# Kernel optimization log

Hardware: AMD Instinct MI355X
Metric: run time of the kernel (lower is better)

The kernel has to match this reference:

```python
import jax, jax.numpy as jnp
import numpy as np
from jax import lax

# Poincare ball, curvature c = 1.0 (geoopt default for CustomPoincare)
SQRT_C = 1.0
BALL_EPS = 1e-3   # projx margin (geoopt-style)
MIN_NORM = 1e-7
BN_EPS = 1e-5


def _norm(x):
    # norm over channel (last) dim, clamped away from 0
    return jnp.maximum(jnp.linalg.norm(x, axis=-1, keepdims=True), MIN_NORM)


def projx(x):
    # clip points back inside the ball of radius (1-eps)/sqrt(c)
    maxnorm = (1.0 - BALL_EPS) / SQRT_C
    n = _norm(x)
    return x * jnp.minimum(1.0, maxnorm / n)


def expmap0(v):
    # exp map at the origin: tanh(sqrt(c)||v||) * v / (sqrt(c)||v||)
    n = _norm(v)
    return projx(jnp.tanh(SQRT_C * n) * v / (SQRT_C * n))


def logmap0(x):
    # log map at the origin: artanh(sqrt(c)||x||) * x / (sqrt(c)||x||)
    n = _norm(x)
    t = jnp.minimum(SQRT_C * n, 1.0 - 1e-5)
    return jnp.arctanh(t) * x / (SQRT_C * n)


def setup_inputs() -> dict:
    key = jax.random.key(0)
    k0, k1 = jax.random.split(key)
    B, C_in, H, W, C_out = 16, 3, 224, 224, 64
    x = jax.random.normal(k0, (B, C_in, H, W), dtype=jnp.float32)
    # Kaiming-ish init for the 3x3 stem conv, HWIO layout
    fan_in = 3 * 3 * C_in
    conv_w = jax.random.normal(k1, (3, 3, C_in, C_out), dtype=jnp.float32) * np.float32(np.sqrt(2.0 / fan_in))
    conv_b = jnp.zeros((C_out,), dtype=jnp.float32)
    bn_gamma = jnp.ones((C_out,), dtype=jnp.float32)
    bn_beta = jnp.zeros((C_out,), dtype=jnp.float32)
    return {"x": x, "conv_w": conv_w, "conv_b": conv_b,
            "bn_gamma": bn_gamma, "bn_beta": bn_beta}


def reference(x, conv_w, conv_b, bn_gamma, bn_beta):
    # x: [B, C, H, W] -> NHWC (channel-last points on the Poincare ball)
    h = jnp.transpose(x, (0, 2, 3, 1))
    h = projx(h)

    # --- PoincareConv2d: tangent-space 3x3 conv (log0 -> conv+bias -> exp0) ---
    u = logmap0(h)
    u = lax.conv_general_dilated(
        u, conv_w, window_strides=(1, 1), padding="SAME",
        dimension_numbers=("NHWC", "HWIO", "NHWC"))
    u = u + conv_b
    h = expmap0(u)

    # --- PoincareBatchNorm2d: tangent-space BN over (B,H,W) per channel ---
    u = logmap0(h)
    mean = jnp.mean(u, axis=(0, 1, 2), keepdims=True)
    var = jnp.var(u, axis=(0, 1, 2), keepdims=True)
    u = (u - mean) * lax.rsqrt(var + BN_EPS) * bn_gamma + bn_beta
    h = expmap0(u)

    # --- PoincareTangentReLU ---
    h = expmap0(jax.nn.relu(logmap0(h)))
    return h  # [B, H, W, C_out]
```

## Files before the change

### kernel.cpp

```cpp
#include <hip/hip_runtime.h>
#include <math.h>

#define B_ 16
#define H_ 224
#define W_ 224
#define HP_ 226
#define WP_ 226
#define CIN_ 3
#define COUT_ 64
#define NPIX_ (B_ * H_ * W_)
#define NPAD_ (B_ * HP_ * WP_)
#define NBLK_ (NPIX_ / 256)
#define MAXNORM_ 0.999f
#define MINN_ 1e-7f
#define TCL_ (1.0f - 1e-5f)
#define LCLAMP_ 3.8002012f
#define BN_EPS_ 1e-5f
#define NF_ ((float)NPIX_)
#define PADW2_ 36

typedef float v4f __attribute__((ext_vector_type(4)));

struct Acc {
  v4f v0, v1, v2, v3, v4, v5, v6, v7, v8, v9, v10, v11, v12, v13, v14, v15;
};

#define EACH16(X) X(0) X(1) X(2) X(3) X(4) X(5) X(6) X(7) \
                  X(8) X(9) X(10) X(11) X(12) X(13) X(14) X(15)
#define EACH8LO(X) X(0) X(1) X(2) X(3) X(4) X(5) X(6) X(7)
#define EACH8HI(X) X(8) X(9) X(10) X(11) X(12) X(13) X(14) X(15)

__global__ void k0_transform(const float* __restrict__ x, float4* __restrict__ u0p) {
  int idx = blockIdx.x * 256 + threadIdx.x;
  if (idx >= NPAD_) return;
  int b = idx / (HP_ * WP_);
  int r = idx % (HP_ * WP_);
  int yp = r / WP_, xp = r % WP_;
  float4 o = make_float4(0.f, 0.f, 0.f, 0.f);
  if (yp >= 1 && yp <= H_ && xp >= 1 && xp <= W_) {
    const float* xb = x + (size_t)b * (CIN_ * H_ * W_) + (size_t)(yp - 1) * W_ + (xp - 1);
    float v0 = xb[0];
    float v1 = xb[H_ * W_];
    float v2 = xb[2 * H_ * W_];
    float n = sqrtf(fmaf(v0, v0, fmaf(v1, v1, v2 * v2)));
    float ncl = fmaxf(n, MINN_);
    float s = fminf(1.0f, MAXNORM_ / ncl);
    float p0 = v0 * s, p1 = v1 * s, p2 = v2 * s;
    float np_ = fmaxf(sqrtf(fmaf(p0, p0, fmaf(p1, p1, p2 * p2))), MINN_);
    float t = fminf(np_, TCL_);
    float ath = 0.5f * __logf(__fdividef(1.0f + t, 1.0f - t));
    float f = __fdividef(ath, np_);
    o.x = p0 * f; o.y = p1 * f; o.z = p2 * f;
  }
  u0p[idx] = o;
}

__device__ __forceinline__ void conv_clamp(const float4* __restrict__ u0p,
                                           const float* __restrict__ wgt,
                                           const float* __restrict__ bias,
                                           int pix, Acc& a) {
  int b = pix / (H_ * W_);
  int r = pix % (H_ * W_);
  int y = r / W_, x = r % W_;
  const float4* base = u0p + ((size_t)b * HP_ + y) * WP_ + x;
  const v4f* b4 = (const v4f*)bias;
#define INIT(i) a.v##i = b4[i];
  EACH16(INIT)
#undef INIT
#define FMA_X(i) a.v##i += in.x * wp[i];
#define FMA_Y(i) a.v##i += in.y * wp[16 + i];
#define FMA_Z(i) a.v##i += in.z * wp[32 + i];
#define TAP(t) { float4 in = base[((t) / 3) * WP_ + ((t) % 3)];              \
                 const v4f* wp = (const v4f*)(wgt + (t) * 3 * COUT_);        \
                 EACH16(FMA_X) EACH16(FMA_Y) EACH16(FMA_Z) }
  TAP(0) TAP(1) TAP(2) TAP(3) TAP(4) TAP(5) TAP(6) TAP(7) TAP(8)
#undef TAP
#undef FMA_X
#undef FMA_Y
#undef FMA_Z
  v4f s2 = (v4f)0.0f;
#define SQ(i) s2 += a.v##i * a.v##i;
  EACH16(SQ)
#undef SQ
  float n2 = s2.x + s2.y + s2.z + s2.w;
  float n = sqrtf(n2);
  float sc = (n > LCLAMP_) ? (LCLAMP_ / n) : 1.0f;
#define SCL(i) a.v##i *= sc;
  EACH16(SCL)
}

__global__ void __launch_bounds__(256, 4)
k1_stats(const float4* __restrict__ u0p, const float* __restrict__ wgt,
         const float* __restrict__ bias, float* __restrict__ partials) {
  int pix = blockIdx.x * 256 + threadIdx.x;
  Acc a;
  conv_clamp(u0p, wgt, bias, pix, a);

  __shared__ __align__(16) float stg[4 * 64 * PADW2_];
  __shared__ float red[512];
  int lane = threadIdx.x & 63, wid = threadIdx.x >> 6;
  float* row = stg + (size_t)(wid * 64 + lane) * PADW2_;
  int c = lane & 31, half = lane >> 5;
  const float* col = stg + ((size_t)wid * 64 + half * 32) * PADW2_ + c;

#define STGA(i) *(v4f*)(row + 4 * (i)) = a.v##i;
  EACH8LO(STGA)
#undef STGA
  __builtin_amdgcn_wave_barrier();
  float sA0 = 0.f, sA1 = 0.f, qA0 = 0.f, qA1 = 0.f;
#pragma unroll
  for (int p = 0; p < 32; p += 2) {
    float a0 = col[(p + 0) * PADW2_];
    float a1 = col[(p + 1) * PADW2_];
    sA0 += a0; qA0 = fmaf(a0, a0, qA0);
    sA1 += a1; qA1 = fmaf(a1, a1, qA1);
  }
  float sA = sA0 + sA1, qA = qA0 + qA1;
  __builtin_amdgcn_wave_barrier();

#define STGB(i) *(v4f*)(row + 4 * ((i) - 8)) = a.v##i;
  EACH8HI(STGB)
#undef STGB
  __builtin_amdgcn_wave_barrier();
  float sB0 = 0.f, sB1 = 0.f, qB0 = 0.f, qB1 = 0.f;
#pragma unroll
  for (int p = 0; p < 32; p += 2) {
    float a0 = col[(p + 0) * PADW2_];
    float a1 = col[(p + 1) * PADW2_];
    sB0 += a0; qB0 = fmaf(a0, a0, qB0);
    sB1 += a1; qB1 = fmaf(a1, a1, qB1);
  }
  float sB = sB0 + sB1, qB = qB0 + qB1;

  sA += __shfl_xor(sA, 32, 64);  qA += __shfl_xor(qA, 32, 64);
  sB += __shfl_xor(sB, 32, 64);  qB += __shfl_xor(qB, 32, 64);

  if (lane < 32) {
    red[0 * 128 + wid * 32 + c] = sA;
    red[1 * 128 + wid * 32 + c] = sB;
    red[2 * 128 + wid * 32 + c] = qA;
    red[3 * 128 + wid * 32 + c] = qB;
  }
  __syncthreads();
  int tid = threadIdx.x;
  if (tid < 128) {
    int base = (tid >> 5) * 128 + (tid & 31);
    float tot = red[base] + red[base + 32] + red[base + 64] + red[base + 96];
    partials[(size_t)blockIdx.x * 128 + tid] = tot;
  }
}

__global__ void k2_finalize(const float* __restrict__ partials, const float* __restrict__ gamma,
                            float* __restrict__ stats) {
  int c = blockIdx.x;
  int t = threadIdx.x;
  float s = 0.f, q = 0.f;
  for (int i = t; i < NBLK_; i += 256) {
    s += partials[(size_t)i * 128 + c];
    q += partials[(size_t)i * 128 + 64 + c];
  }
  __shared__ float ls[256], lq[256];
  ls[t] = s; lq[t] = q;
  __syncthreads();
#pragma unroll
  for (int off = 128; off > 0; off >>= 1) {
    if (t < off) { ls[t] += ls[t + off]; lq[t] += lq[t + off]; }
    __syncthreads();
  }
  if (t == 0) {
    float mean = ls[0] / NF_;
    float msq  = lq[0] / NF_;
    float var = msq - mean * mean;
    stats[c] = mean;
    stats[64 + c] = gamma[c] / sqrtf(var + BN_EPS_);
  }
}

__global__ void __launch_bounds__(256, 4)
k3_final(const float4* __restrict__ u0p, const float* __restrict__ wgt,
         const float* __restrict__ bias, const float* __restrict__ stats,
         const float* __restrict__ beta, float* __restrict__ out) {
  int pix = blockIdx.x * 256 + threadIdx.x;
  Acc a;
  conv_clamp(u0p, wgt, bias, pix, a);
  const v4f* mean4 = (const v4f*)stats;
  const v4f* rg4   = (const v4f*)(stats + 64);
  const v4f* beta4 = (const v4f*)beta;
  v4f s2 = (v4f)0.0f;
#define BN(i) { a.v##i = (a.v##i - mean4[i]) * rg4[i] + beta4[i]; s2 += a.v##i * a.v##i; }
  EACH16(BN)
#undef BN
  float nv2 = s2.x + s2.y + s2.z + s2.w;
  float nv = sqrtf(nv2);
  float sv = (nv > LCLAMP_) ? (LCLAMP_ / nv) : 1.0f;
  v4f z2 = (v4f)0.0f;
#define RELU(i) { v4f r = a.v##i * sv;                                      \
                  r.x = fmaxf(r.x, 0.f); r.y = fmaxf(r.y, 0.f);             \
                  r.z = fmaxf(r.z, 0.f); r.w = fmaxf(r.w, 0.f);             \
                  a.v##i = r; z2 += r * r; }
  EACH16(RELU)
#undef RELU
  float nw2 = z2.x + z2.y + z2.z + z2.w;
  float nw = fmaxf(sqrtf(nw2), MINN_);
  float e2 = __expf(2.0f * nw);
  float th = 1.0f - __fdividef(2.0f, e2 + 1.0f);
  float se = __fdividef(th, nw);
  float clip = fminf(1.0f, MAXNORM_ / fmaxf(th, MINN_));
  float fs = se * clip;

  __shared__ __align__(16) float stg[4 * 64 * PADW2_];
  int lane = threadIdx.x & 63, wid = threadIdx.x >> 6;
  float* row = stg + (size_t)(wid * 64 + lane) * PADW2_;
  int pr8 = lane >> 3, qi = lane & 7;
  const float* rb = stg + (size_t)wid * 64 * PADW2_ + pr8 * PADW2_ + qi * 4;
  v4f* outw = (v4f*)out + ((size_t)blockIdx.x * 256 + wid * 64) * 16;

#define STGA(i) *(v4f*)(row + 4 * (i)) = a.v##i * fs;
  EACH8LO(STGA)
#undef STGA
  __builtin_amdgcn_wave_barrier();
#pragma unroll
  for (int j = 0; j < 8; j++) {
    v4f v = *(const v4f*)(rb + j * 8 * PADW2_);
    __builtin_nontemporal_store(v, outw + (j * 8 + pr8) * 16 + qi);
  }
  __builtin_amdgcn_wave_barrier();

#define STGB(i) *(v4f*)(row + 4 * ((i) - 8)) = a.v##i * fs;
  EACH8HI(STGB)
#undef STGB
  __builtin_amdgcn_wave_barrier();
#pragma unroll
  for (int j = 0; j < 8; j++) {
    v4f v = *(const v4f*)(rb + j * 8 * PADW2_);
    __builtin_nontemporal_store(v, outw + (j * 8 + pr8) * 16 + 8 + qi);
  }
}

extern "C" void kernel_launch(void* const* d_in, const int* in_sizes, int n_in,
                              void* d_out, int out_size, void* d_ws, size_t ws_size,
                              hipStream_t stream) {
  const float* x     = (const float*)d_in[0];
  const float* wgt   = (const float*)d_in[1];
  const float* bias  = (const float*)d_in[2];
  const float* gamma = (const float*)d_in[3];
  const float* beta  = (const float*)d_in[4];
  float* out = (float*)d_out;

  char* ws = (char*)d_ws;
  float4* u0p      = (float4*)ws;
  float*  partials = (float*)(ws + (size_t)NPAD_ * 16);
  float*  stats    = (float*)(ws + (size_t)NPAD_ * 16 + (size_t)NBLK_ * 128 * 4);

  hipLaunchKernelGGL(k0_transform, dim3((NPAD_ + 255) / 256), dim3(256), 0, stream, x, u0p);
  hipLaunchKernelGGL(k1_stats,     dim3(NBLK_),               dim3(256), 0, stream, u0p, wgt, bias, partials);
  hipLaunchKernelGGL(k2_finalize,  dim3(64),                  dim3(256), 0, stream, partials, gamma, stats);
  hipLaunchKernelGGL(k3_final,     dim3(NBLK_),               dim3(256), 0, stream, u0p, wgt, bias, stats, beta, out);
}
```

Measured before the change: 307.9 us.

## Materialize clamped conv output in workspace instead of recomputing conv in final pass

The stats kernel now writes the clamped tangent-space conv result to a workspace buffer, and a new final kernel reads that buffer rather than re-running the 3x3 conv. The stats reduction is also reworked to read from the transposed staging layout with vector shuffles. This swaps repeated conv compute for an extra 205MB write plus read of global memory. A fallback keeps the recompute path when the workspace is too small.

```diff
diff --git a/kernel.cpp b/kernel.cpp
--- a/kernel.cpp
+++ b/kernel.cpp
@@ -89,63 +89,77 @@
   EACH16(SCL)
 }
 
+__device__ __forceinline__ v4f vshfl_xor(v4f v, int m) {
+  v4f r;
+  r.x = __shfl_xor(v.x, m, 64);
+  r.y = __shfl_xor(v.y, m, 64);
+  r.z = __shfl_xor(v.z, m, 64);
+  r.w = __shfl_xor(v.w, m, 64);
+  return r;
+}
+
+template <bool STORE_T>
 __global__ void __launch_bounds__(256, 4)
 k1_stats(const float4* __restrict__ u0p, const float* __restrict__ wgt,
-         const float* __restrict__ bias, float* __restrict__ partials) {
+         const float* __restrict__ bias, float* __restrict__ tbuf,
+         float* __restrict__ partials) {
   int pix = blockIdx.x * 256 + threadIdx.x;
   Acc a;
   conv_clamp(u0p, wgt, bias, pix, a);
 
   __shared__ __align__(16) float stg[4 * 64 * PADW2_];
-  __shared__ float red[512];
+  __shared__ float red_s[256], red_q[256];
   int lane = threadIdx.x & 63, wid = threadIdx.x >> 6;
   float* row = stg + (size_t)(wid * 64 + lane) * PADW2_;
-  int c = lane & 31, half = lane >> 5;
-  const float* col = stg + ((size_t)wid * 64 + half * 32) * PADW2_ + c;
+  int pr8 = lane >> 3, qi = lane & 7;
+  const float* rb = stg + (size_t)wid * 64 * PADW2_ + pr8 * PADW2_ + qi * 4;
+  v4f* outw = (v4f*)tbuf + ((size_t)blockIdx.x * 256 + wid * 64) * 16;
 
 #define STGA(i) *(v4f*)(row + 4 * (i)) = a.v##i;
   EACH8LO(STGA)
 #undef STGA
   __builtin_amdgcn_wave_barrier();
-  float sA0 = 0.f, sA1 = 0.f, qA0 = 0.f, qA1 = 0.f;
-#pragma unroll
-  for (int p = 0; p < 32; p += 2) {
-    float a0 = col[(p + 0) * PADW2_];
-    float a1 = col[(p + 1) * PADW2_];
-    sA0 += a0; qA0 = fmaf(a0, a0, qA0);
-    sA1 += a1; qA1 = fmaf(a1, a1, qA1);
-  }
-  float sA = sA0 + sA1, qA = qA0 + qA1;
+  v4f sA = (v4f)0.0f, qA = (v4f)0.0f;
+#pragma unroll
+  for (int j = 0; j < 8; j++) {
+    v4f v = *(const v4f*)(rb + j * 8 * PADW2_);
+    if (STORE_T) __builtin_nontemporal_store(v, outw + (j * 8 + pr8) * 16 + qi);
+    sA += v; qA += v * v;
+  }
+  sA += vshfl_xor(sA, 8);  qA += vshfl_xor(qA, 8);
+  sA += vshfl_xor(sA, 16); qA += vshfl_xor(qA, 16);
+  sA += vshfl_xor(sA, 32); qA += vshfl_xor(qA, 32);
+  if (lane < 8) {
+    *(v4f*)&red_s[wid * 32 + qi * 4] = sA;
+    *(v4f*)&red_q[wid * 32 + qi * 4] = qA;
+  }
   __builtin_amdgcn_wave_barrier();
 
 #define STGB(i) *(v4f*)(row + 4 * ((i) - 8)) = a.v##i;
   EACH8HI(STGB)
 #undef STGB
   __builtin_amdgcn_wave_barrier();
-  float sB0 = 0.f, sB1 = 0.f, qB0 = 0.f, qB1 = 0.f;
-#pragma unroll
-  for (int p = 0; p < 32; p += 2) {
-    float a0 = col[(p + 0) * PADW2_];
-    float a1 = col[(p + 1) * PADW2_];
-    sB0 += a0; qB0 = fmaf(a0, a0, qB0);
-    sB1 += a1; qB1 = fmaf(a1, a1, qB1);
-  }
-  float sB = sB0 + sB1, qB = qB0 + qB1;
-
-  sA += __shfl_xor(sA, 32, 64);  qA += __shfl_xor(qA, 32, 64);
-  sB += __shfl_xor(sB, 32, 64);  qB += __shfl_xor(qB, 32, 64);
-
-  if (lane < 32) {
-    red[0 * 128 + wid * 32 + c] = sA;
-    red[1 * 128 + wid * 32 + c] = sB;
-    red[2 * 128 + wid * 32 + c] = qA;
-    red[3 * 128 + wid * 32 + c] = qB;
+  v4f sB = (v4f)0.0f, qB = (v4f)0.0f;
+#pragma unroll
+  for (int j = 0; j < 8; j++) {
+    v4f v = *(const v4f*)(rb + j * 8 * PADW2_);
+    if (STORE_T) __builtin_nontemporal_store(v, outw + (j * 8 + pr8) * 16 + 8 + qi);
+    sB += v; qB += v * v;
+  }
+  sB += vshfl_xor(sB, 8);  qB += vshfl_xor(qB, 8);
+  sB += vshfl_xor(sB, 16); qB += vshfl_xor(qB, 16);
+  sB += vshfl_xor(sB, 32); qB += vshfl_xor(qB, 32);
+  if (lane < 8) {
+    *(v4f*)&red_s[128 + wid * 32 + qi * 4] = sB;
+    *(v4f*)&red_q[128 + wid * 32 + qi * 4] = qB;
   }
   __syncthreads();
   int tid = threadIdx.x;
   if (tid < 128) {
-    int base = (tid >> 5) * 128 + (tid & 31);
-    float tot = red[base] + red[base + 32] + red[base + 64] + red[base + 96];
+    int c = tid & 63;
+    int base = (c >> 5) * 128 + (c & 31);
+    const float* rr = (tid < 64) ? red_s : red_q;
+    float tot = rr[base] + rr[base + 32] + rr[base + 64] + rr[base + 96];
     partials[(size_t)blockIdx.x * 128 + tid] = tot;
   }
 }
@@ -176,13 +190,9 @@
   }
 }
 
-__global__ void __launch_bounds__(256, 4)
-k3_final(const float4* __restrict__ u0p, const float* __restrict__ wgt,
-         const float* __restrict__ bias, const float* __restrict__ stats,
-         const float* __restrict__ beta, float* __restrict__ out) {
-  int pix = blockIdx.x * 256 + threadIdx.x;
-  Acc a;
-  conv_clamp(u0p, wgt, bias, pix, a);
+__device__ __forceinline__ void bn_relu_exp_store(Acc& a, const float* __restrict__ stats,
+                                                  const float* __restrict__ beta,
+                                                  float* __restrict__ out) {
   const v4f* mean4 = (const v4f*)stats;
   const v4f* rg4   = (const v4f*)(stats + 64);
   const v4f* beta4 = (const v4f*)beta;
@@ -225,7 +235,6 @@
     __builtin_nontemporal_store(v, outw + (j * 8 + pr8) * 16 + qi);
   }
   __builtin_amdgcn_wave_barrier();
-
 #define STGB(i) *(v4f*)(row + 4 * ((i) - 8)) = a.v##i * fs;
   EACH8HI(STGB)
 #undef STGB
@@ -235,6 +244,28 @@
     v4f v = *(const v4f*)(rb + j * 8 * PADW2_);
     __builtin_nontemporal_store(v, outw + (j * 8 + pr8) * 16 + 8 + qi);
   }
+}
+
+__global__ void __launch_bounds__(256, 4)
+k3_from_t(const float* __restrict__ tbuf, const float* __restrict__ stats,
+          const float* __restrict__ beta, float* __restrict__ out) {
+  int pix = blockIdx.x * 256 + threadIdx.x;
+  const v4f* tp = (const v4f*)tbuf + (size_t)pix * 16;
+  Acc a;
+#define LOADT(i) a.v##i = tp[i];
+  EACH16(LOADT)
+#undef LOADT
+  bn_relu_exp_store(a, stats, beta, out);
+}
+
+__global__ void __launch_bounds__(256, 4)
+k3_fused(const float4* __restrict__ u0p, const float* __restrict__ wgt,
+         const float* __restrict__ bias, const float* __restrict__ stats,
+         const float* __restrict__ beta, float* __restrict__ out) {
+  int pix = blockIdx.x * 256 + threadIdx.x;
+  Acc a;
+  conv_clamp(u0p, wgt, bias, pix, a);
+  bn_relu_exp_store(a, stats, beta, out);
 }
 
 extern "C" void kernel_launch(void* const* d_in, const int* in_sizes, int n_in,
@@ -251,9 +282,18 @@
   float4* u0p      = (float4*)ws;
   float*  partials = (float*)(ws + (size_t)NPAD_ * 16);
   float*  stats    = (float*)(ws + (size_t)NPAD_ * 16 + (size_t)NBLK_ * 128 * 4);
+  size_t  t_off    = (size_t)NPAD_ * 16 + (size_t)NBLK_ * 128 * 4 + 512;
+  float*  tbuf     = (float*)(ws + t_off);
+  bool have_t = ws_size >= t_off + (size_t)NPIX_ * COUT_ * 4;
 
   hipLaunchKernelGGL(k0_transform, dim3((NPAD_ + 255) / 256), dim3(256), 0, stream, x, u0p);
-  hipLaunchKernelGGL(k1_stats,     dim3(NBLK_),               dim3(256), 0, stream, u0p, wgt, bias, partials);
-  hipLaunchKernelGGL(k2_finalize,  dim3(64),                  dim3(256), 0, stream, partials, gamma, stats);
-  hipLaunchKernelGGL(k3_final,     dim3(NBLK_),               dim3(256), 0, stream, u0p, wgt, bias, stats, beta, out);
-}
+  if (have_t) {
+    hipLaunchKernelGGL((k1_stats<true>),  dim3(NBLK_), dim3(256), 0, stream, u0p, wgt, bias, tbuf, partials);
+    hipLaunchKernelGGL(k2_finalize,       dim3(64),    dim3(256), 0, stream, partials, gamma, stats);
+    hipLaunchKernelGGL(k3_from_t,         dim3(NBLK_), dim3(256), 0, stream, tbuf, stats, beta, out);
+  } else {
+    hipLaunchKernelGGL((k1_stats<false>), dim3(NBLK_), dim3(256), 0, stream, u0p, wgt, bias, tbuf, partials);
+    hipLaunchKernelGGL(k2_finalize,       dim3(64),    dim3(256), 0, stream, partials, gamma, stats);
+    hipLaunchKernelGGL(k3_fused,          dim3(NBLK_), dim3(256), 0, stream, u0p, wgt, bias, stats, beta, out);
+  }
+}
```

New measurement: 366.0 us. 18.8% more time.

## Map output channels to lanes and stage row chunks in LDS for conv

Applied to the files above, without the earlier changes.

The conv+BN kernels switch from one pixel per thread holding all 64 channels to one channel per lane. Each wave processes half an image row, staging 3x58 input pixels in LDS and keeping the 27 weights in registers. Channel norms are computed with cross-lane butterfly shuffles. Per-wave partial stats replace the LDS transpose reduction, and output is written as coalesced 64-channel rows without staging. This cuts register pressure and LDS transposes, but adds many shuffles per pixel and makes each wave run a long serial loop over 112 pixels.

```diff
diff --git a/kernel.cpp b/kernel.cpp
--- a/kernel.cpp
+++ b/kernel.cpp
@@ -6,29 +6,17 @@
 #define W_ 224
 #define HP_ 226
 #define WP_ 226
-#define CIN_ 3
-#define COUT_ 64
 #define NPIX_ (B_ * H_ * W_)
 #define NPAD_ (B_ * HP_ * WP_)
-#define NBLK_ (NPIX_ / 256)
+#define NROWS_ (B_ * H_ * 2)
+#define NBLKC_ (NROWS_ / 4)
 #define MAXNORM_ 0.999f
 #define MINN_ 1e-7f
 #define TCL_ (1.0f - 1e-5f)
 #define LCLAMP_ 3.8002012f
 #define BN_EPS_ 1e-5f
 #define NF_ ((float)NPIX_)
-#define PADW2_ 36
-
-typedef float v4f __attribute__((ext_vector_type(4)));
-
-struct Acc {
-  v4f v0, v1, v2, v3, v4, v5, v6, v7, v8, v9, v10, v11, v12, v13, v14, v15;
-};
-
-#define EACH16(X) X(0) X(1) X(2) X(3) X(4) X(5) X(6) X(7) \
-                  X(8) X(9) X(10) X(11) X(12) X(13) X(14) X(15)
-#define EACH8LO(X) X(0) X(1) X(2) X(3) X(4) X(5) X(6) X(7)
-#define EACH8HI(X) X(8) X(9) X(10) X(11) X(12) X(13) X(14) X(15)
+
 
 __global__ void k0_transform(const float* __restrict__ x, float4* __restrict__ u0p) {
   int idx = blockIdx.x * 256 + threadIdx.x;
@@ -38,7 +26,7 @@
   int yp = r / WP_, xp = r % WP_;
   float4 o = make_float4(0.f, 0.f, 0.f, 0.f);
   if (yp >= 1 && yp <= H_ && xp >= 1 && xp <= W_) {
-    const float* xb = x + (size_t)b * (CIN_ * H_ * W_) + (size_t)(yp - 1) * W_ + (xp - 1);
+    const float* xb = x + (size_t)b * (3 * H_ * W_) + (size_t)(yp - 1) * W_ + (xp - 1);
     float v0 = xb[0];
     float v1 = xb[H_ * W_];
     float v2 = xb[2 * H_ * W_];
@@ -55,99 +43,86 @@
   u0p[idx] = o;
 }
 
-__device__ __forceinline__ void conv_clamp(const float4* __restrict__ u0p,
-                                           const float* __restrict__ wgt,
-                                           const float* __restrict__ bias,
-                                           int pix, Acc& a) {
-  int b = pix / (H_ * W_);
-  int r = pix % (H_ * W_);
-  int y = r / W_, x = r % W_;
-  const float4* base = u0p + ((size_t)b * HP_ + y) * WP_ + x;
-  const v4f* b4 = (const v4f*)bias;
-#define INIT(i) a.v##i = b4[i];
-  EACH16(INIT)
-#undef INIT
-#define FMA_X(i) a.v##i += in.x * wp[i];
-#define FMA_Y(i) a.v##i += in.y * wp[16 + i];
-#define FMA_Z(i) a.v##i += in.z * wp[32 + i];
-#define TAP(t) { float4 in = base[((t) / 3) * WP_ + ((t) % 3)];              \
-                 const v4f* wp = (const v4f*)(wgt + (t) * 3 * COUT_);        \
-                 EACH16(FMA_X) EACH16(FMA_Y) EACH16(FMA_Z) }
-  TAP(0) TAP(1) TAP(2) TAP(3) TAP(4) TAP(5) TAP(6) TAP(7) TAP(8)
-#undef TAP
-#undef FMA_X
-#undef FMA_Y
-#undef FMA_Z
-  v4f s2 = (v4f)0.0f;
-#define SQ(i) s2 += a.v##i * a.v##i;
-  EACH16(SQ)
-#undef SQ
-  float n2 = s2.x + s2.y + s2.z + s2.w;
-  float n = sqrtf(n2);
-  float sc = (n > LCLAMP_) ? (LCLAMP_ / n) : 1.0f;
-#define SCL(i) a.v##i *= sc;
-  EACH16(SCL)
-}
+#define DEFCOL(n) float4 n##0, n##1, n##2;
+#define LDCOL(n, j) { n##0 = ub[(j)]; n##1 = ub[58 + (j)]; n##2 = ub[116 + (j)]; }
+#define CPYCOL(d, s) { d##0 = s##0; d##1 = s##1; d##2 = s##2; }
+
+#define C3(acc, X, d)                                                        \
+  acc = fmaf((X##0).x, w_[((0 * 3 + (d)) * 3) + 0], acc);                    \
+  acc = fmaf((X##0).y, w_[((0 * 3 + (d)) * 3) + 1], acc);                    \
+  acc = fmaf((X##0).z, w_[((0 * 3 + (d)) * 3) + 2], acc);                    \
+  acc = fmaf((X##1).x, w_[((1 * 3 + (d)) * 3) + 0], acc);                    \
+  acc = fmaf((X##1).y, w_[((1 * 3 + (d)) * 3) + 1], acc);                    \
+  acc = fmaf((X##1).z, w_[((1 * 3 + (d)) * 3) + 2], acc);                    \
+  acc = fmaf((X##2).x, w_[((2 * 3 + (d)) * 3) + 0], acc);                    \
+  acc = fmaf((X##2).y, w_[((2 * 3 + (d)) * 3) + 1], acc);                    \
+  acc = fmaf((X##2).z, w_[((2 * 3 + (d)) * 3) + 2], acc);
+
+#define BFLY1(x) {                                                           \
+  x += __shfl_xor(x, 1, 64);  x += __shfl_xor(x, 2, 64);                     \
+  x += __shfl_xor(x, 4, 64);  x += __shfl_xor(x, 8, 64);                     \
+  x += __shfl_xor(x, 16, 64); x += __shfl_xor(x, 32, 64); }
+#define BFLY2(x, y) {                                                        \
+  x += __shfl_xor(x, 1, 64);  y += __shfl_xor(y, 1, 64);                     \
+  x += __shfl_xor(x, 2, 64);  y += __shfl_xor(y, 2, 64);                     \
+  x += __shfl_xor(x, 4, 64);  y += __shfl_xor(y, 4, 64);                     \
+  x += __shfl_xor(x, 8, 64);  y += __shfl_xor(y, 8, 64);                     \
+  x += __shfl_xor(x, 16, 64); y += __shfl_xor(y, 16, 64);                    \
+  x += __shfl_xor(x, 32, 64); y += __shfl_xor(y, 32, 64); }
+
+#define CONV_SETUP()                                                         \
+  int tid = threadIdx.x, lane = tid & 63, wid = tid >> 6;                    \
+  int id = blockIdx.x * 4 + wid;                                             \
+  int b = id / (H_ * 2); int rem = id % (H_ * 2);                            \
+  int y = rem >> 1; int hx0 = (rem & 1) * 112;                               \
+  float w_[27];                                                              \
+  _Pragma("unroll")                                                          \
+  for (int k = 0; k < 27; k++) w_[k] = wgt[k * 64 + lane];                   \
+  float bi = bias[lane];                                                     \
+  const float4* ubase = u0p + ((size_t)b * HP_ + y) * WP_;                   \
+  float4* ub = U[wid];
+
+#define STAGE_CHUNK(c0)                                                      \
+  if (lane < 58) {                                                           \
+    ub[lane]       = ubase[(c0) + lane];                                     \
+    ub[58 + lane]  = ubase[WP_ + (c0) + lane];                               \
+    ub[116 + lane] = ubase[2 * WP_ + (c0) + lane];                           \
+  }                                                                          \
+  __asm__ volatile("s_waitcnt lgkmcnt(0)" ::: "memory");                     \
+  __builtin_amdgcn_wave_barrier();
 
 __global__ void __launch_bounds__(256, 4)
 k1_stats(const float4* __restrict__ u0p, const float* __restrict__ wgt,
          const float* __restrict__ bias, float* __restrict__ partials) {
-  int pix = blockIdx.x * 256 + threadIdx.x;
-  Acc a;
-  conv_clamp(u0p, wgt, bias, pix, a);
-
-  __shared__ __align__(16) float stg[4 * 64 * PADW2_];
-  __shared__ float red[512];
-  int lane = threadIdx.x & 63, wid = threadIdx.x >> 6;
-  float* row = stg + (size_t)(wid * 64 + lane) * PADW2_;
-  int c = lane & 31, half = lane >> 5;
-  const float* col = stg + ((size_t)wid * 64 + half * 32) * PADW2_ + c;
-
-#define STGA(i) *(v4f*)(row + 4 * (i)) = a.v##i;
-  EACH8LO(STGA)
-#undef STGA
-  __builtin_amdgcn_wave_barrier();
-  float sA0 = 0.f, sA1 = 0.f, qA0 = 0.f, qA1 = 0.f;
+  __shared__ float4 U[4][176];
+  CONV_SETUP()
+  float s = 0.f, q = 0.f;
+
+#define K1PX(A, B, C) {                                                      \
+    float acc = bi; C3(acc, A, 0) C3(acc, B, 1) C3(acc, C, 2)                \
+    float n2 = acc * acc; BFLY1(n2)                                          \
+    float n = sqrtf(n2);                                                     \
+    float sc = (n > LCLAMP_) ? __fdividef(LCLAMP_, n) : 1.0f;                \
+    float tt = acc * sc;                                                     \
+    s += tt; q = fmaf(tt, tt, q); }
+
 #pragma unroll
-  for (int p = 0; p < 32; p += 2) {
-    float a0 = col[(p + 0) * PADW2_];
-    float a1 = col[(p + 1) * PADW2_];
-    sA0 += a0; qA0 = fmaf(a0, a0, qA0);
-    sA1 += a1; qA1 = fmaf(a1, a1, qA1);
-  }
-  float sA = sA0 + sA1, qA = qA0 + qA1;
-  __builtin_amdgcn_wave_barrier();
-
-#define STGB(i) *(v4f*)(row + 4 * ((i) - 8)) = a.v##i;
-  EACH8HI(STGB)
-#undef STGB
-  __builtin_amdgcn_wave_barrier();
-  float sB0 = 0.f, sB1 = 0.f, qB0 = 0.f, qB1 = 0.f;
-#pragma unroll
-  for (int p = 0; p < 32; p += 2) {
-    float a0 = col[(p + 0) * PADW2_];
-    float a1 = col[(p + 1) * PADW2_];
-    sB0 += a0; qB0 = fmaf(a0, a0, qB0);
-    sB1 += a1; qB1 = fmaf(a1, a1, qB1);
-  }
-  float sB = sB0 + sB1, qB = qB0 + qB1;
-
-  sA += __shfl_xor(sA, 32, 64);  qA += __shfl_xor(qA, 32, 64);
-  sB += __shfl_xor(sB, 32, 64);  qB += __shfl_xor(qB, 32, 64);
-
-  if (lane < 32) {
-    red[0 * 128 + wid * 32 + c] = sA;
-    red[1 * 128 + wid * 32 + c] = sB;
-    red[2 * 128 + wid * 32 + c] = qA;
-    red[3 * 128 + wid * 32 + c] = qB;
-  }
-  __syncthreads();
-  int tid = threadIdx.x;
-  if (tid < 128) {
-    int base = (tid >> 5) * 128 + (tid & 31);
-    float tot = red[base] + red[base + 32] + red[base + 64] + red[base + 96];
-    partials[(size_t)blockIdx.x * 128 + tid] = tot;
-  }
+  for (int ch = 0; ch < 2; ch++) {
+    int c0 = hx0 + 56 * ch;
+    STAGE_CHUNK(c0)
+    DEFCOL(A) DEFCOL(B) DEFCOL(C) DEFCOL(D)
+    LDCOL(A, 0) LDCOL(B, 1)
+    for (int g = 0; g < 28; g++) {
+      LDCOL(C, 2 * g + 2) LDCOL(D, 2 * g + 3)
+      K1PX(A, B, C)
+      K1PX(B, C, D)
+      CPYCOL(A, C) CPYCOL(B, D)
+    }
+    __builtin_amdgcn_wave_barrier();
+  }
+#undef K1PX
+  partials[(size_t)id * 128 + lane] = s;
+  partials[(size_t)id * 128 + 64 + lane] = q;
 }
 
 __global__ void k2_finalize(const float* __restrict__ partials, const float* __restrict__ gamma,
@@ -155,7 +130,7 @@
   int c = blockIdx.x;
   int t = threadIdx.x;
   float s = 0.f, q = 0.f;
-  for (int i = t; i < NBLK_; i += 256) {
+  for (int i = t; i < NROWS_; i += 256) {
     s += partials[(size_t)i * 128 + c];
     q += partials[(size_t)i * 128 + 64 + c];
   }
@@ -180,61 +155,47 @@
 k3_final(const float4* __restrict__ u0p, const float* __restrict__ wgt,
          const float* __restrict__ bias, const float* __restrict__ stats,
          const float* __restrict__ beta, float* __restrict__ out) {
-  int pix = blockIdx.x * 256 + threadIdx.x;
-  Acc a;
-  conv_clamp(u0p, wgt, bias, pix, a);
-  const v4f* mean4 = (const v4f*)stats;
-  const v4f* rg4   = (const v4f*)(stats + 64);
-  const v4f* beta4 = (const v4f*)beta;
-  v4f s2 = (v4f)0.0f;
-#define BN(i) { a.v##i = (a.v##i - mean4[i]) * rg4[i] + beta4[i]; s2 += a.v##i * a.v##i; }
-  EACH16(BN)
-#undef BN
-  float nv2 = s2.x + s2.y + s2.z + s2.w;
-  float nv = sqrtf(nv2);
-  float sv = (nv > LCLAMP_) ? (LCLAMP_ / nv) : 1.0f;
-  v4f z2 = (v4f)0.0f;
-#define RELU(i) { v4f r = a.v##i * sv;                                      \
-                  r.x = fmaxf(r.x, 0.f); r.y = fmaxf(r.y, 0.f);             \
-                  r.z = fmaxf(r.z, 0.f); r.w = fmaxf(r.w, 0.f);             \
-                  a.v##i = r; z2 += r * r; }
-  EACH16(RELU)
-#undef RELU
-  float nw2 = z2.x + z2.y + z2.z + z2.w;
-  float nw = fmaxf(sqrtf(nw2), MINN_);
-  float e2 = __expf(2.0f * nw);
-  float th = 1.0f - __fdividef(2.0f, e2 + 1.0f);
-  float se = __fdividef(th, nw);
-  float clip = fminf(1.0f, MAXNORM_ / fmaxf(th, MINN_));
-  float fs = se * clip;
-
-  __shared__ __align__(16) float stg[4 * 64 * PADW2_];
-  int lane = threadIdx.x & 63, wid = threadIdx.x >> 6;
-  float* row = stg + (size_t)(wid * 64 + lane) * PADW2_;
-  int pr8 = lane >> 3, qi = lane & 7;
-  const float* rb = stg + (size_t)wid * 64 * PADW2_ + pr8 * PADW2_ + qi * 4;
-  v4f* outw = (v4f*)out + ((size_t)blockIdx.x * 256 + wid * 64) * 16;
-
-#define STGA(i) *(v4f*)(row + 4 * (i)) = a.v##i * fs;
-  EACH8LO(STGA)
-#undef STGA
-  __builtin_amdgcn_wave_barrier();
+  __shared__ float4 U[4][176];
+  CONV_SETUP()
+  float mn = stats[lane], rgv = stats[64 + lane];
+  float bt = beta[lane];
+
+#define K3PX(A, B, C, px) {                                                  \
+    float acc = bi; C3(acc, A, 0) C3(acc, B, 1) C3(acc, C, 2)                \
+    float n2 = acc * acc; BFLY1(n2)                                          \
+    float n = sqrtf(n2);                                                     \
+    float sc = (n > LCLAMP_) ? __fdividef(LCLAMP_, n) : 1.0f;                \
+    float u3 = (acc * sc - mn) * rgv + bt;                                   \
+    float a2 = u3 * u3;                                                      \
+    float rl = fmaxf(u3, 0.f);                                               \
+    float r2 = rl * rl;                                                      \
+    BFLY2(a2, r2)                                                            \
+    float nv = sqrtf(a2);                                                    \
+    float sv = (nv > LCLAMP_) ? __fdividef(LCLAMP_, nv) : 1.0f;              \
+    float nw = fmaxf(sv * sqrtf(r2), MINN_);                                 \
+    float e2 = __expf(2.0f * nw);                                            \
+    float th = 1.0f - __fdividef(2.0f, e2 + 1.0f);                           \
+    float se = __fdividef(th, nw);                                           \
+    float clip = fminf(1.0f, MAXNORM_ / fmaxf(th, MINN_));                   \
+    float g = se * clip * sv;                                                \
+    obase[(size_t)(px) * 64 + lane] = rl * g; }
+
 #pragma unroll
-  for (int j = 0; j < 8; j++) {
-    v4f v = *(const v4f*)(rb + j * 8 * PADW2_);
-    __builtin_nontemporal_store(v, outw + (j * 8 + pr8) * 16 + qi);
-  }
-  __builtin_amdgcn_wave_barrier();
-
-#define STGB(i) *(v4f*)(row + 4 * ((i) - 8)) = a.v##i * fs;
-  EACH8HI(STGB)
-#undef STGB
-  __builtin_amdgcn_wave_barrier();
-#pragma unroll
-  for (int j = 0; j < 8; j++) {
-    v4f v = *(const v4f*)(rb + j * 8 * PADW2_);
-    __builtin_nontemporal_store(v, outw + (j * 8 + pr8) * 16 + 8 + qi);
-  }
+  for (int ch = 0; ch < 2; ch++) {
+    int c0 = hx0 + 56 * ch;
+    STAGE_CHUNK(c0)
+    float* obase = out + ((size_t)((b * H_ + y) * W_) + hx0 + 56 * ch) * 64;
+    DEFCOL(A) DEFCOL(B) DEFCOL(C) DEFCOL(D)
+    LDCOL(A, 0) LDCOL(B, 1)
+    for (int g2 = 0; g2 < 28; g2++) {
+      LDCOL(C, 2 * g2 + 2) LDCOL(D, 2 * g2 + 3)
+      K3PX(A, B, C, 2 * g2)
+      K3PX(B, C, D, 2 * g2 + 1)
+      CPYCOL(A, C) CPYCOL(B, D)
+    }
+    __builtin_amdgcn_wave_barrier();
+  }
+#undef K3PX
 }
 
 extern "C" void kernel_launch(void* const* d_in, const int* in_sizes, int n_in,
@@ -250,10 +211,10 @@
   char* ws = (char*)d_ws;
   float4* u0p      = (float4*)ws;
   float*  partials = (float*)(ws + (size_t)NPAD_ * 16);
-  float*  stats    = (float*)(ws + (size_t)NPAD_ * 16 + (size_t)NBLK_ * 128 * 4);
+  float*  stats    = (float*)(ws + (size_t)NPAD_ * 16 + (size_t)NROWS_ * 128 * 4);
 
   hipLaunchKernelGGL(k0_transform, dim3((NPAD_ + 255) / 256), dim3(256), 0, stream, x, u0p);
-  hipLaunchKernelGGL(k1_stats,     dim3(NBLK_),               dim3(256), 0, stream, u0p, wgt, bias, partials);
+  hipLaunchKernelGGL(k1_stats,     dim3(NBLKC_),              dim3(256), 0, stream, u0p, wgt, bias, partials);
   hipLaunchKernelGGL(k2_finalize,  dim3(64),                  dim3(256), 0, stream, partials, gamma, stats);
-  hipLaunchKernelGGL(k3_final,     dim3(NBLK_),               dim3(256), 0, stream, u0p, wgt, bias, stats, beta, out);
-}
+  hipLaunchKernelGGL(k3_final,     dim3(NBLKC_),              dim3(256), 0, stream, u0p, wgt, bias, stats, beta, out);
+}
```

Result: slower. 521.7 us (+69.4%).
